# Optimization experiments

Measured on AMD Instinct MI355X. Metric: run time of the kernel, lower is better.

Reference implementation:

```python
import jax, jax.numpy as jnp
import numpy as np

VAR0, VAR1 = 0.1, 0.2
THRESHOLD = 0.35
NEGPOS_RATIO = 7
LOW_GT_THRESH = 0.2  # match() filters GT whose best prior IoU < 0.2


def setup_inputs() -> dict:
    key = jax.random.key(0)
    ks = jax.random.split(key, 8)
    B, P, G = 16, 43008, 128
    loc_data = jax.random.normal(ks[0], (B, P, 4), jnp.float32)
    conf_data = jax.random.normal(ks[1], (B, P, 2), jnp.float32)
    landm_data = jax.random.normal(ks[2], (B, P, 10), jnp.float32)
    # priors in cxcywh form, positive sizes
    pc = jax.random.uniform(ks[3], (P, 2), jnp.float32)
    pwh = jax.random.uniform(ks[4], (P, 2), jnp.float32, minval=0.02, maxval=0.32)
    priors = jnp.concatenate([pc, pwh], axis=1)
    # targets: valid xyxy boxes + 10 landmark coords + label (face=1)
    ctr = jax.random.uniform(ks[5], (B, G, 2), jnp.float32, minval=0.2, maxval=0.8)
    wh = jax.random.uniform(ks[6], (B, G, 2), jnp.float32, minval=0.05, maxval=0.3)
    boxes = jnp.concatenate([ctr - wh / 2, ctr + wh / 2], axis=-1)
    landms = jax.random.uniform(ks[7], (B, G, 10), jnp.float32)
    labels = jnp.ones((B, G, 1), jnp.float32)
    targets = jnp.concatenate([boxes, landms, labels], axis=-1)
    return {"loc_data": loc_data, "conf_data": conf_data, "landm_data": landm_data,
            "priors": priors, "targets": targets}


def point_form(priors):
    return jnp.concatenate([priors[:, :2] - priors[:, 2:] / 2,
                            priors[:, :2] + priors[:, 2:] / 2], axis=1)


def jaccard(a, b):  # a: [G,4] xyxy, b: [P,4] xyxy -> [G,P]
    lt = jnp.maximum(a[:, None, :2], b[None, :, :2])
    rb = jnp.minimum(a[:, None, 2:], b[None, :, 2:])
    wh = jnp.clip(rb - lt, 0.0)
    inter = wh[..., 0] * wh[..., 1]
    area_a = (a[:, 2] - a[:, 0]) * (a[:, 3] - a[:, 1])
    area_b = (b[:, 2] - b[:, 0]) * (b[:, 3] - b[:, 1])
    return inter / (area_a[:, None] + area_b[None, :] - inter)


def encode(matched, priors):  # matched xyxy [P,4], priors cxcywh [P,4]
    g_cxcy = (matched[:, :2] + matched[:, 2:]) / 2 - priors[:, :2]
    g_cxcy = g_cxcy / (VAR0 * priors[:, 2:])
    g_wh = jnp.log((matched[:, 2:] - matched[:, :2]) / priors[:, 2:]) / VAR1
    return jnp.concatenate([g_cxcy, g_wh], axis=1)


def encode_landm(matched, priors):  # matched [P,10], priors [P,4]
    m = matched.reshape(-1, 5, 2)
    g = (m - priors[:, None, :2]) / (VAR0 * priors[:, None, 2:])
    return g.reshape(-1, 10)


def match_one(truths, labels, landms, priors):
    G = truths.shape[0]
    overlaps = jaccard(truths, point_form(priors))  # [G, P]
    best_prior_overlap = overlaps.max(axis=1)       # [G]
    best_prior_idx = overlaps.argmax(axis=1)        # [G]
    valid = best_prior_overlap >= LOW_GT_THRESH
    any_valid = jnp.any(valid)
    best_truth_overlap = overlaps.max(axis=0)       # [P]
    best_truth_idx = overlaps.argmax(axis=0)        # [P]
    # index_fill_(0, best_prior_idx_filter, 2): ensure each valid GT keeps its best prior
    fill_val = jnp.where(valid, 2.0, best_truth_overlap[best_prior_idx])
    best_truth_overlap = best_truth_overlap.at[best_prior_idx].set(fill_val)
    # best_truth_idx[best_prior_idx[j]] = j for all j
    best_truth_idx = best_truth_idx.at[best_prior_idx].set(jnp.arange(G))
    matches = truths[best_truth_idx]                       # [P,4]
    conf = labels[best_truth_idx].astype(jnp.int32)        # [P]
    conf = jnp.where(best_truth_overlap < THRESHOLD, 0, conf)
    conf = jnp.where(any_valid, conf, 0)  # no valid GT -> all background
    loc = encode(matches, priors)
    landm = encode_landm(landms[best_truth_idx], priors)
    return loc, conf, landm


def smooth_l1(x):
    ax = jnp.abs(x)
    return jnp.where(ax < 1.0, 0.5 * ax * ax, ax - 0.5)


def reference(loc_data, conf_data, landm_data, priors, targets):
    truths = targets[..., :4]
    landms = targets[..., 4:14]
    labels = targets[..., 14]
    loc_t, conf_t, landm_t = jax.vmap(
        lambda t, l, lm: match_one(t, l, lm, priors))(truths, labels, landms)

    # landmark loss over positives
    pos1 = conf_t > 0
    N1 = jnp.maximum(pos1.sum().astype(jnp.float32), 1.0)
    loss_landm = jnp.sum(smooth_l1(landm_data - landm_t) * pos1[..., None])

    # localization loss over positives
    pos = conf_t != 0
    num_pos = pos.sum(axis=1, keepdims=True)  # [B,1]
    loss_l = jnp.sum(smooth_l1(loc_data - loc_t) * pos[..., None])

    # hard negative mining on per-prior CE loss
    lse = jax.scipy.special.logsumexp(conf_data, axis=-1)  # [B,P]
    gathered = jnp.take_along_axis(conf_data, conf_t[..., None], axis=-1)[..., 0]
    ce_all = lse - gathered                                # [B,P] per-prior CE
    mine = jnp.where(pos, 0.0, ce_all)
    loss_idx = jnp.argsort(-mine, axis=1)
    idx_rank = jnp.argsort(loss_idx, axis=1)
    num_neg = jnp.clip(NEGPOS_RATIO * num_pos, None, pos.shape[1] - 1)
    neg = idx_rank < num_neg
    sel = pos | neg
    loss_c = jnp.sum(jnp.where(sel, ce_all, 0.0))

    N = jnp.maximum(num_pos.sum().astype(jnp.float32), 1.0)
    return loss_l / N, loss_c / N, loss_landm / N1
```

## Files before the change

### kernel.cpp

```cpp
#include <hip/hip_runtime.h>
#include <stdint.h>


#define GC 8
#define PPI 4

__device__ __forceinline__ float sl1(float x) {
  float a = fabsf(x);
  return a < 1.f ? 0.5f * a * a : a - 0.5f;
}

__device__ __forceinline__ double dwave(double v) {
#pragma unroll
  for (int o = 32; o; o >>= 1) v += __shfl_down(v, o);
  return v;
}

__global__ __launch_bounds__(256) void k_mm(
    const float* __restrict__ priors, const float* __restrict__ targets,
    const float* __restrict__ loc, const float* __restrict__ conf,
    const float* __restrict__ lm, float* __restrict__ bto,
    int* __restrict__ bti, unsigned long long* __restrict__ bp,
    float* __restrict__ mine, double* __restrict__ pll,
    double* __restrict__ pllm, double* __restrict__ plc,
    double* __restrict__ msum, int* __restrict__ pnp, int P, int G, int NIOU,
    int PTI, int NGC, int PC) {
  int tid = threadIdx.x;
  __shared__ char smem[16384];
  __shared__ float4 sgt[128];
  __shared__ float sga[128];

  if ((int)blockIdx.x < NIOU) {
    float* st = (float*)smem;
    double* rs = (double*)(smem + 7680);
    int* ri = (int*)(smem + 7808);
    int b = blockIdx.x / PTI, tile = blockIdx.x % PTI;
    int base = tile * (256 * PPI);
    for (int i = tid; i < G * 15; i += 256)
      st[i] = targets[(size_t)b * G * 15 + i];
    for (int g = tid; g < G; g += 256) {
      const float* t = targets + ((size_t)b * G + g) * 15;
      float x1 = t[0], y1 = t[1], x2 = t[2], y2 = t[3];
      sgt[g] = make_float4(x1, y1, x2, y2);
      sga[g] = (x2 - x1) * (y2 - y1);
    }
    __syncthreads();

    float px1[PPI], py1[PPI], px2[PPI], py2[PPI], pa[PPI];
    float bi[PPI], sb[PPI];
    int bidx[PPI];
#pragma unroll
    for (int k = 0; k < PPI; ++k) {
      int p = base + tid + k * 256;
      int pl = p < P ? p : P - 1;
      float4 pr = ((const float4*)priors)[pl];
      px1[k] = pr.x - pr.z * 0.5f; py1[k] = pr.y - pr.w * 0.5f;
      px2[k] = pr.x + pr.z * 0.5f; py2[k] = pr.y + pr.w * 0.5f;
      pa[k] = pr.z * pr.w;
      bi[k] = 0.f; sb[k] = 1.f; bidx[k] = 0;
    }

#define IOU_BODY(T, A, GG)                                                 \
  {                                                                        \
    float iw = fminf(T.z, px2[k]) - fmaxf(T.x, px1[k]);                    \
    float ih = fminf(T.w, py2[k]) - fmaxf(T.y, py1[k]);                    \
    float inter = fmaxf(iw, 0.f) * ih;                                     \
    float S = A + pa[k];                                                   \
    if (inter * sb[k] > bi[k] * S) { bi[k] = inter; sb[k] = S; bidx[k] = GG; } \
  }
    for (int g = 0; g < G; g += 4) {
      float4 T0 = sgt[g], T1 = sgt[g + 1], T2 = sgt[g + 2], T3 = sgt[g + 3];
      float A0 = sga[g], A1 = sga[g + 1], A2 = sga[g + 2], A3 = sga[g + 3];
#pragma unroll
      for (int k = 0; k < PPI; ++k) {
        IOU_BODY(T0, A0, g)
        IOU_BODY(T1, A1, g + 1)
        IOU_BODY(T2, A2, g + 2)
        IOU_BODY(T3, A3, g + 3)
      }
    }
#undef IOU_BODY

    double ll = 0, llm = 0, lc = 0, ms = 0;
    int np = 0;
#pragma unroll
    for (int k = 0; k < PPI; ++k) {
      int p = base + tid + k * 256;
      if (p < P) {
        size_t idx = (size_t)b * P + p;
        float ov = bi[k] / (sb[k] - bi[k]);
        int ti = bidx[k];
        bto[idx] = ov;
        bti[idx] = ti;
        bool pos = ov >= 0.35f;
        float2 c = ((const float2*)conf)[idx];
        float mx = fmaxf(c.x, c.y);
        float dd = fabsf(c.x - c.y);
        float lse = mx + logf(1.f + expf(-dd));
        float ce = lse - (pos ? c.y : c.x);
        float mv = pos ? 0.f : ce;
        mine[idx] = mv;
        ms += (double)mv;
        if (pos) {
          np++;
          lc += (double)ce;
          float4 pr = ((const float4*)priors)[p];
          const float* t = st + ti * 15;
          float rz = 1.f / pr.z, rw = 1.f / pr.w;
          float rdx = 10.f * rz, rdy = 10.f * rw;
          float gx = ((t[0] + t[2]) * 0.5f - pr.x) * rdx;
          float gy = ((t[1] + t[3]) * 0.5f - pr.y) * rdy;
          float gw = logf((t[2] - t[0]) * rz) * 5.0f;
          float gh = logf((t[3] - t[1]) * rw) * 5.0f;
          float4 ld = ((const float4*)loc)[idx];
          ll += (double)(sl1(ld.x - gx) + sl1(ld.y - gy) + sl1(ld.z - gw) +
                         sl1(ld.w - gh));
          const float2* lmd = (const float2*)lm + idx * 5;
          float s = 0.f;
#pragma unroll
          for (int j = 0; j < 5; ++j) {
            float2 lv = lmd[j];
            float ex = (t[4 + 2 * j] - pr.x) * rdx;
            float ey = (t[5 + 2 * j] - pr.y) * rdy;
            s += sl1(lv.x - ex) + sl1(lv.y - ey);
          }
          llm += (double)s;
        }
      }
    }

    ll = dwave(ll); llm = dwave(llm); lc = dwave(lc); ms = dwave(ms);
#pragma unroll
    for (int o = 32; o; o >>= 1) np += __shfl_down(np, o);
    int lane = tid & 63, wid = tid >> 6;
    if (lane == 0) {
      rs[wid] = ll; rs[4 + wid] = llm; rs[8 + wid] = lc; rs[12 + wid] = ms;
      ri[wid] = np;
    }
    __syncthreads();
    if (tid == 0) {
      pll[blockIdx.x] = rs[0] + rs[1] + rs[2] + rs[3];
      pllm[blockIdx.x] = rs[4] + rs[5] + rs[6] + rs[7];
      plc[blockIdx.x] = rs[8] + rs[9] + rs[10] + rs[11];
      msum[blockIdx.x] = rs[12] + rs[13] + rs[14] + rs[15];
      pnp[blockIdx.x] = ri[0] + ri[1] + ri[2] + ri[3];
    }
  } else {
    unsigned long long* sred = (unsigned long long*)smem;
    int bc = blockIdx.x - NIOU;
    int pc = bc % PC;
    int gcb = (bc / PC) % NGC;
    int b = bc / (PC * NGC);
    int g0 = gcb * GC;

    if (tid < GC) {
      int g = g0 + tid;
      float4 v = make_float4(0.f, 0.f, 0.f, 0.f);
      if (g < G) {
        const float* t = targets + ((size_t)b * G + g) * 15;
        v = make_float4(t[0], t[1], t[2], t[3]);
      }
      sgt[tid] = v;
    }
    __syncthreads();

    float gx1[GC], gy1[GC], gx2[GC], gy2[GC], ga[GC];
#pragma unroll
    for (int j = 0; j < GC; ++j) {
      float4 T = sgt[j];
      gx1[j] = T.x; gy1[j] = T.y; gx2[j] = T.z; gy2[j] = T.w;
      ga[j] = (T.z - T.x) * (T.w - T.y);
    }

    int chunk = (P + PC - 1) / PC;
    int ps = pc * chunk;
    int pe = ps + chunk; if (pe > P) pe = P;
    int count = pe - ps;

    float bi[GC], sb[GC];
    unsigned bpp[GC];
#pragma unroll
    for (int j = 0; j < GC; ++j) { bi[j] = 0.f; sb[j] = 1.f; bpp[j] = (unsigned)(ps + tid); }

#define BP_BODY(X1, Y1, X2, Y2, AR, PP)                                     \
  {                                                                         \
    float iw = fminf(gx2[j], X2) - fmaxf(gx1[j], X1);                       \
    float ih = fminf(gy2[j], Y2) - fmaxf(gy1[j], Y1);                       \
    float inter = fmaxf(iw, 0.f) * ih;                                      \
    float S = ga[j] + AR;                                                   \
    if (inter * sb[j] > bi[j] * S) { bi[j] = inter; sb[j] = S; bpp[j] = (unsigned)PP; } \
  }
    for (int i = tid; i < count; i += 1024) {
      int p0 = ps + i;
      int i1 = i + 256, i2 = i + 512, i3 = i + 768;
      int p1 = (i1 < count) ? ps + i1 : p0;
      int p2 = (i2 < count) ? ps + i2 : p0;
      int p3 = (i3 < count) ? ps + i3 : p0;
      float4 q0 = ((const float4*)priors)[p0];
      float4 q1 = ((const float4*)priors)[p1];
      float4 q2 = ((const float4*)priors)[p2];
      float4 q3 = ((const float4*)priors)[p3];
      float ax1 = q0.x - q0.z * 0.5f, ay1 = q0.y - q0.w * 0.5f;
      float ax2 = q0.x + q0.z * 0.5f, ay2 = q0.y + q0.w * 0.5f;
      float aa = q0.z * q0.w;
      float bx1 = q1.x - q1.z * 0.5f, by1 = q1.y - q1.w * 0.5f;
      float bx2 = q1.x + q1.z * 0.5f, by2 = q1.y + q1.w * 0.5f;
      float ba = q1.z * q1.w;
      float cx1 = q2.x - q2.z * 0.5f, cy1 = q2.y - q2.w * 0.5f;
      float cx2 = q2.x + q2.z * 0.5f, cy2 = q2.y + q2.w * 0.5f;
      float ca = q2.z * q2.w;
      float dx1 = q3.x - q3.z * 0.5f, dy1 = q3.y - q3.w * 0.5f;
      float dx2 = q3.x + q3.z * 0.5f, dy2 = q3.y + q3.w * 0.5f;
      float da = q3.z * q3.w;
#pragma unroll
      for (int j = 0; j < GC; ++j) {
        BP_BODY(ax1, ay1, ax2, ay2, aa, p0)
        BP_BODY(bx1, by1, bx2, by2, ba, p1)
        BP_BODY(cx1, cy1, cx2, cy2, ca, p2)
        BP_BODY(dx1, dy1, dx2, dy2, da, p3)
      }
    }
#undef BP_BODY

#pragma unroll
    for (int j = 0; j < GC; ++j) {
      float iou = bi[j] / (sb[j] - bi[j]);
      unsigned long long pk =
          ((unsigned long long)__float_as_uint(iou) << 32) | (unsigned)(~bpp[j]);
      sred[j * 256 + tid] = pk;
    }
    __syncthreads();
    {
      int j = tid >> 5, s = tid & 31;
      unsigned long long m = sred[j * 256 + s];
#pragma unroll
      for (int t = 1; t < 8; ++t) {
        unsigned long long v = sred[j * 256 + s + t * 32];
        if (v > m) m = v;
      }
      __syncthreads();
      sred[j * 256 + s] = m;
    }
    __syncthreads();
    if (tid < GC) {
      unsigned long long m = sred[tid * 256];
      for (int s = 1; s < 32; ++s) {
        unsigned long long v = sred[tid * 256 + s];
        if (v > m) m = v;
      }
      int g = g0 + tid;
      if (g < G) atomicMax(&bp[(size_t)b * G + g], m);
    }
  }
}

__global__ void k_fix(const unsigned long long* __restrict__ bp,
                      const float* __restrict__ bto, const int* __restrict__ bti,
                      const float* __restrict__ conf, const float* __restrict__ loc,
                      const float* __restrict__ lm, const float* __restrict__ priors,
                      const float* __restrict__ targets, float* __restrict__ mine,
                      int* __restrict__ anyv, double* __restrict__ dacc,
                      int* __restrict__ dnpb, int P, int G) {
  int b = blockIdx.x, g = threadIdx.x;
  __shared__ unsigned spp[128];
  __shared__ double sd[128 * 4];
  __shared__ int si[128];

  unsigned long long m = bp[(size_t)b * G + g];
  unsigned pp = ~(unsigned)m;
  float val = __uint_as_float((unsigned)(m >> 32));
  spp[g] = pp;
  bool valid = val >= 0.2f;
  int av = __syncthreads_or(valid ? 1 : 0);
  if (g == 0) anyv[b] = av;

  bool win = true;
  for (int g2 = g + 1; g2 < G; ++g2)
    if (spp[g2] == pp) { win = false; break; }

  double dll = 0, dllm = 0, dlc = 0, dms = 0;
  int dnp = 0;
  if (win) {
    size_t idx = (size_t)b * P + pp;
    float ov_o = bto[idx];
    int ti_o = bti[idx];
    float ov_n = valid ? 2.0f : ov_o;
    int ti_n = g;
    bool pos_o = ov_o >= 0.35f, pos_n = ov_n >= 0.35f;

    float2 c = ((const float2*)conf)[idx];
    float mx = fmaxf(c.x, c.y);
    float dd = fabsf(c.x - c.y);
    float lse = mx + logf(1.f + expf(-dd));
    float ce_o = lse - (pos_o ? c.y : c.x);
    float ce_n = lse - (pos_n ? c.y : c.x);
    float mv_o = mine[idx];
    float mv_n = pos_n ? 0.f : ce_n;
    if (mv_n != mv_o) mine[idx] = mv_n;
    dms = (double)mv_n - (double)mv_o;
    dnp = (pos_n ? 1 : 0) - (pos_o ? 1 : 0);
    dlc = (pos_n ? (double)ce_n : 0.0) - (pos_o ? (double)ce_o : 0.0);

    if (pos_o || pos_n) {
      float4 pr = ((const float4*)priors)[pp];
      float rz = 1.f / pr.z, rw = 1.f / pr.w;
      float rdx = 10.f * rz, rdy = 10.f * rw;
      float4 ld = ((const float4*)loc)[idx];
      const float2* lmd = (const float2*)lm + idx * 5;
      float2 lv[5];
#pragma unroll
      for (int j = 0; j < 5; ++j) lv[j] = lmd[j];
      for (int pass = 0; pass < 2; ++pass) {
        bool act = pass ? pos_n : pos_o;
        int ti = pass ? ti_n : ti_o;
        if (!act) continue;
        const float* t = targets + ((size_t)b * G + ti) * 15;
        float gx = ((t[0] + t[2]) * 0.5f - pr.x) * rdx;
        float gy = ((t[1] + t[3]) * 0.5f - pr.y) * rdy;
        float gw = logf((t[2] - t[0]) * rz) * 5.0f;
        float gh = logf((t[3] - t[1]) * rw) * 5.0f;
        double l = (double)(sl1(ld.x - gx) + sl1(ld.y - gy) +
                            sl1(ld.z - gw) + sl1(ld.w - gh));
        float s = 0.f;
#pragma unroll
        for (int j = 0; j < 5; ++j) {
          float ex = (t[4 + 2 * j] - pr.x) * rdx;
          float ey = (t[5 + 2 * j] - pr.y) * rdy;
          s += sl1(lv[j].x - ex) + sl1(lv[j].y - ey);
        }
        if (pass) { dll += l; dllm += (double)s; }
        else { dll -= l; dllm -= (double)s; }
      }
    }
  }
  sd[g] = dll; sd[128 + g] = dllm; sd[256 + g] = dlc; sd[384 + g] = dms;
  si[g] = dnp;
  __syncthreads();
  for (int off = 64; off; off >>= 1) {
    if (g < off) {
      sd[g] += sd[g + off]; sd[128 + g] += sd[128 + g + off];
      sd[256 + g] += sd[256 + g + off]; sd[384 + g] += sd[384 + g + off];
      si[g] += si[g + off];
    }
    __syncthreads();
  }
  if (g == 0) {
    dacc[b * 4 + 0] = sd[0]; dacc[b * 4 + 1] = sd[128];
    dacc[b * 4 + 2] = sd[256]; dacc[b * 4 + 3] = sd[384];
    dnpb[b] = si[0];
  }
}

__global__ __launch_bounds__(1024) void k_tail(
    const int* __restrict__ pnp, const double* __restrict__ msum,
    const double* __restrict__ pll, const double* __restrict__ pllm,
    const double* __restrict__ plc, const double* __restrict__ dacc,
    const int* __restrict__ dnpb, const int* __restrict__ anyv,
    const float* __restrict__ mine, int* __restrict__ num_pos,
    double* __restrict__ pllb, double* __restrict__ pllmb,
    double* __restrict__ plcb, double* __restrict__ pfs_b, int P, int PTI) {
  int b = blockIdx.x, tid = threadIdx.x;
  __shared__ double rs[16 * 5];
  __shared__ int ris[16];
  __shared__ unsigned S[1024];
  __shared__ unsigned hs[2048];
  __shared__ int spf1, sk1, spf21, sk2;
  __shared__ unsigned stb;
  __shared__ double stie;

  double a = 0, cc = 0, d = 0, ms = 0;
  int n = 0;
  for (int i = tid; i < PTI; i += 1024) {
    int ix = b * PTI + i;
    a += pll[ix]; cc += pllm[ix]; d += plc[ix]; ms += msum[ix]; n += pnp[ix];
  }
  a = dwave(a); cc = dwave(cc); d = dwave(d); ms = dwave(ms);
#pragma unroll
  for (int o = 32; o; o >>= 1) n += __shfl_down(n, o);
  int lane = tid & 63, wid = tid >> 6;
  if (lane == 0) {
    rs[wid] = a; rs[16 + wid] = cc; rs[32 + wid] = d; rs[48 + wid] = ms;
    ris[wid] = n;
  }
  __syncthreads();
  int npos = 0;
  double A = 0, C = 0, D = 0, MS = 0;
  if (tid == 0) {
    for (int i = 0; i < 16; ++i) {
      A += rs[i]; C += rs[16 + i]; D += rs[32 + i]; MS += rs[48 + i];
      npos += ris[i];
    }
    A += dacc[b * 4 + 0]; C += dacc[b * 4 + 1]; D += dacc[b * 4 + 2];
    MS += dacc[b * 4 + 3];
    npos += dnpb[b];
    if (!anyv[b]) { A = 0; C = 0; D = 0; npos = 0; }
    num_pos[b] = npos;
    pllb[b] = A; pllmb[b] = C; plcb[b] = D;
    ris[0] = npos;
    rs[48] = MS;
  }
  __syncthreads();
  npos = ris[0];
  MS = rs[48];

  long long k = 7LL * (long long)npos;
  long long cap = P - 1;
  if (k <= 0) {
    if (tid == 0) pfs_b[b] = 0.0;
    return;
  }
  if (k >= cap) {
    if (tid == 0) pfs_b[b] = MS;
    return;
  }

  const float* mrow = mine + (size_t)b * P;
  hs[tid] = 0;
  __syncthreads();
  for (int base = 0; base < P; base += 4096) {
    int i0 = base + tid;
    int i1 = i0 + 1024, i2 = i0 + 2048, i3 = i0 + 3072;
    unsigned b0 = (i0 < P) ? __float_as_uint(mrow[i0]) : 0xFFFFFFFFu;
    unsigned b1 = (i1 < P) ? __float_as_uint(mrow[i1]) : 0xFFFFFFFFu;
    unsigned b2 = (i2 < P) ? __float_as_uint(mrow[i2]) : 0xFFFFFFFFu;
    unsigned b3 = (i3 < P) ? __float_as_uint(mrow[i3]) : 0xFFFFFFFFu;
    if (b0 != 0xFFFFFFFFu) atomicAdd(&hs[b0 >> 21], 1u);
    if (b1 != 0xFFFFFFFFu) atomicAdd(&hs[b1 >> 21], 1u);
    if (b2 != 0xFFFFFFFFu) atomicAdd(&hs[b2 >> 21], 1u);
    if (b3 != 0xFFFFFFFFu) atomicAdd(&hs[b3 >> 21], 1u);
  }
  __syncthreads();
  {
    S[tid] = hs[tid];
    __syncthreads();
    for (int off = 1; off < 1024; off <<= 1) {
      unsigned add = (tid + off < 1024) ? S[tid + off] : 0;
      __syncthreads();
      S[tid] += add;
      __syncthreads();
    }
    int cnt = __syncthreads_count((long long)S[tid] >= k);
    int seg = cnt - 1;
    if (tid == seg) {
      long long cum = (seg + 1 < 1024) ? (long long)S[seg + 1] : 0;
      spf1 = seg;
      sk1 = (int)(k - cum);
    }
  }
  __syncthreads();
  int pf = spf1;

  hs[tid] = 0; hs[tid + 1024] = 0;
  __syncthreads();
  for (int base = 0; base < P; base += 4096) {
    int i0 = base + tid;
    int i1 = i0 + 1024, i2 = i0 + 2048, i3 = i0 + 3072;
    unsigned b0 = (i0 < P) ? __float_as_uint(mrow[i0]) : 0u;
    unsigned b1 = (i1 < P) ? __float_as_uint(mrow[i1]) : 0u;
    unsigned b2 = (i2 < P) ? __float_as_uint(mrow[i2]) : 0u;
    unsigned b3 = (i3 < P) ? __float_as_uint(mrow[i3]) : 0u;
    if (i0 < P && (int)(b0 >> 21) == pf) atomicAdd(&hs[(b0 >> 10) & 2047], 1u);
    if (i1 < P && (int)(b1 >> 21) == pf) atomicAdd(&hs[(b1 >> 10) & 2047], 1u);
    if (i2 < P && (int)(b2 >> 21) == pf) atomicAdd(&hs[(b2 >> 10) & 2047], 1u);
    if (i3 < P && (int)(b3 >> 21) == pf) atomicAdd(&hs[(b3 >> 10) & 2047], 1u);
  }
  __syncthreads();
  {
    unsigned h0 = hs[tid * 2], h1v = hs[tid * 2 + 1];
    S[tid] = h0 + h1v;
    __syncthreads();
    for (int off = 1; off < 1024; off <<= 1) {
      unsigned add = (tid + off < 1024) ? S[tid + off] : 0;
      __syncthreads();
      S[tid] += add;
      __syncthreads();
    }
    long long kk = (long long)sk1;
    int cnt = __syncthreads_count((long long)S[tid] >= kk);
    int seg = cnt - 1;
    if (tid == seg) {
      long long cum = (seg + 1 < 1024) ? (long long)S[seg + 1] : 0;
      int bin = seg * 2;
      if (cum + h1v >= kk) bin = seg * 2 + 1;
      else cum += h1v;
      spf21 = (pf << 11) | bin;
      sk2 = (int)(kk - cum);
    }
  }
  __syncthreads();
  int pf21 = spf21;

  hs[tid] = 0;
  __syncthreads();
  for (int base = 0; base < P; base += 4096) {
    int i0 = base + tid;
    int i1 = i0 + 1024, i2 = i0 + 2048, i3 = i0 + 3072;
    unsigned b0 = (i0 < P) ? __float_as_uint(mrow[i0]) : 0u;
    unsigned b1 = (i1 < P) ? __float_as_uint(mrow[i1]) : 0u;
    unsigned b2 = (i2 < P) ? __float_as_uint(mrow[i2]) : 0u;
    unsigned b3 = (i3 < P) ? __float_as_uint(mrow[i3]) : 0u;
    if (i0 < P && (int)(b0 >> 10) == pf21) atomicAdd(&hs[b0 & 1023], 1u);
    if (i1 < P && (int)(b1 >> 10) == pf21) atomicAdd(&hs[b1 & 1023], 1u);
    if (i2 < P && (int)(b2 >> 10) == pf21) atomicAdd(&hs[b2 & 1023], 1u);
    if (i3 < P && (int)(b3 >> 10) == pf21) atomicAdd(&hs[b3 & 1023], 1u);
  }
  __syncthreads();
  {
    S[tid] = hs[tid];
    __syncthreads();
    for (int off = 1; off < 1024; off <<= 1) {
      unsigned add = (tid + off < 1024) ? S[tid + off] : 0;
      __syncthreads();
      S[tid] += add;
      __syncthreads();
    }
    long long kk = (long long)sk2;
    int cnt = __syncthreads_count((long long)S[tid] >= kk);
    int seg = cnt - 1;
    if (tid == seg) {
      long long cum = (seg + 1 < 1024) ? (long long)S[seg + 1] : 0;
      unsigned tb = ((unsigned)pf21 << 10) | (unsigned)seg;
      stb = tb;
      stie = (double)(kk - cum) * (double)__uint_as_float(tb);
    }
  }
  __syncthreads();

  unsigned tb = stb;
  double v = 0.0;
  for (int base = 0; base < P; base += 4096) {
    int i0 = base + tid;
    int i1 = i0 + 1024, i2 = i0 + 2048, i3 = i0 + 3072;
    unsigned b0 = (i0 < P) ? __float_as_uint(mrow[i0]) : 0u;
    unsigned b1 = (i1 < P) ? __float_as_uint(mrow[i1]) : 0u;
    unsigned b2 = (i2 < P) ? __float_as_uint(mrow[i2]) : 0u;
    unsigned b3 = (i3 < P) ? __float_as_uint(mrow[i3]) : 0u;
    if (b0 > tb) v += (double)__uint_as_float(b0);
    if (b1 > tb) v += (double)__uint_as_float(b1);
    if (b2 > tb) v += (double)__uint_as_float(b2);
    if (b3 > tb) v += (double)__uint_as_float(b3);
  }
  v = dwave(v);
  if (lane == 0) rs[wid] = v;
  __syncthreads();
  if (tid == 0) {
    double t = 0;
    for (int i = 0; i < 16; ++i) t += rs[i];
    pfs_b[b] = t + stie;
  }
}

__global__ void k_fin(const double* __restrict__ pllb,
                      const double* __restrict__ pllmb,
                      const double* __restrict__ plcb,
                      const double* __restrict__ pfs_b,
                      const int* __restrict__ num_pos, float* __restrict__ out,
                      int B) {
  if (threadIdx.x == 0) {
    double A = 0, C = 0, D = 0, F = 0, N = 0;
    for (int i = 0; i < B; ++i) {
      A += pllb[i]; C += pllmb[i]; D += plcb[i]; F += pfs_b[i];
      N += (double)num_pos[i];
    }
    if (N < 1.0) N = 1.0;
    out[0] = (float)(A / N);
    out[1] = (float)((D + F) / N);
    out[2] = (float)(C / N);
  }
}

extern "C" void kernel_launch(void* const* d_in, const int* in_sizes, int n_in,
                              void* d_out, int out_size, void* d_ws,
                              size_t ws_size, hipStream_t stream) {
  const float* loc = (const float*)d_in[0];
  const float* conf = (const float*)d_in[1];
  const float* lm = (const float*)d_in[2];
  const float* priors = (const float*)d_in[3];
  const float* targets = (const float*)d_in[4];

  int P = in_sizes[3] / 4;
  int B = in_sizes[0] / (4 * P);
  int G = in_sizes[4] / (15 * B);
  int PTI = (P + 256 * PPI - 1) / (256 * PPI);
  int NIOU = B * PTI;
  int NGC = (G + GC - 1) / GC;
  int PC = 8;
  int NBP = B * NGC * PC;

  char* w = (char*)d_ws;
  size_t off = 0;
  unsigned long long* bp = (unsigned long long*)(w + off);
  off += (size_t)B * G * 8;
  size_t clear_bytes = off;
  off = (off + 255) & ~(size_t)255;
  float* bto = (float*)(w + off);
  off += (size_t)B * P * 4;
  int* bti = (int*)(w + off);
  off += (size_t)B * P * 4;
  float* mine = (float*)(w + off);
  off += (size_t)B * P * 4;
  double* pll = (double*)(w + off);
  off += (size_t)NIOU * 8;
  double* pllm = (double*)(w + off);
  off += (size_t)NIOU * 8;
  double* plc = (double*)(w + off);
  off += (size_t)NIOU * 8;
  double* msum = (double*)(w + off);
  off += (size_t)NIOU * 8;
  int* pnp = (int*)(w + off);
  off += (size_t)NIOU * 4;
  off = (off + 7) & ~(size_t)7;
  double* dacc = (double*)(w + off);
  off += (size_t)B * 4 * 8;
  double* pllb = (double*)(w + off);
  off += (size_t)B * 8;
  double* pllmb = (double*)(w + off);
  off += (size_t)B * 8;
  double* plcb = (double*)(w + off);
  off += (size_t)B * 8;
  double* pfs_b = (double*)(w + off);
  off += (size_t)B * 8;
  int* dnpb = (int*)(w + off);
  off += (size_t)B * 4;
  int* anyv = (int*)(w + off);
  off += (size_t)B * 4;
  int* num_pos = (int*)(w + off);
  off += (size_t)B * 4;

  hipMemsetAsync(d_ws, 0, clear_bytes, stream);

  k_mm<<<NIOU + NBP, 256, 0, stream>>>(priors, targets, loc, conf, lm, bto,
                                       bti, bp, mine, pll, pllm, plc, msum,
                                       pnp, P, G, NIOU, PTI, NGC, PC);
  k_fix<<<B, G, 0, stream>>>(bp, bto, bti, conf, loc, lm, priors, targets,
                             mine, anyv, dacc, dnpb, P, G);
  k_tail<<<B, 1024, 0, stream>>>(pnp, msum, pll, pllm, plc, dacc, dnpb, anyv,
                                 mine, num_pos, pllb, pllmb, plcb, pfs_b, P,
                                 PTI);
  k_fin<<<1, 64, 0, stream>>>(pllb, pllmb, plcb, pfs_b, num_pos,
                              (float*)d_out, B);
}
```

Before: 177.1 us.

## Build top-level histogram in main kernel and compact candidates for radix select

```diff
diff --git a/kernel.cpp b/kernel.cpp
--- a/kernel.cpp
+++ b/kernel.cpp
@@ -21,10 +21,10 @@
     const float* __restrict__ loc, const float* __restrict__ conf,
     const float* __restrict__ lm, float* __restrict__ bto,
     int* __restrict__ bti, unsigned long long* __restrict__ bp,
-    float* __restrict__ mine, double* __restrict__ pll,
-    double* __restrict__ pllm, double* __restrict__ plc,
-    double* __restrict__ msum, int* __restrict__ pnp, int P, int G, int NIOU,
-    int PTI, int NGC, int PC) {
+    float* __restrict__ mine, unsigned* __restrict__ ghist,
+    double* __restrict__ pll, double* __restrict__ pllm,
+    double* __restrict__ plc, double* __restrict__ msum,
+    int* __restrict__ pnp, int P, int G, int NIOU, int PTI, int NGC, int PC) {
   int tid = threadIdx.x;
   __shared__ char smem[16384];
   __shared__ float4 sgt[128];
@@ -34,6 +34,7 @@
     float* st = (float*)smem;
     double* rs = (double*)(smem + 7680);
     int* ri = (int*)(smem + 7808);
+    unsigned* hist = (unsigned*)(smem + 8192);
     int b = blockIdx.x / PTI, tile = blockIdx.x % PTI;
     int base = tile * (256 * PPI);
     for (int i = tid; i < G * 15; i += 256)
@@ -44,6 +45,7 @@
       sgt[g] = make_float4(x1, y1, x2, y2);
       sga[g] = (x2 - x1) * (y2 - y1);
     }
+    for (int i = tid; i < 1024; i += 256) hist[i] = 0;
     __syncthreads();
 
     float px1[PPI], py1[PPI], px2[PPI], py2[PPI], pa[PPI];
@@ -100,6 +102,7 @@
         float ce = lse - (pos ? c.y : c.x);
         float mv = pos ? 0.f : ce;
         mine[idx] = mv;
+        atomicAdd(&hist[__float_as_uint(mv) >> 21], 1u);
         ms += (double)mv;
         if (pos) {
           np++;
@@ -144,6 +147,10 @@
       plc[blockIdx.x] = rs[8] + rs[9] + rs[10] + rs[11];
       msum[blockIdx.x] = rs[12] + rs[13] + rs[14] + rs[15];
       pnp[blockIdx.x] = ri[0] + ri[1] + ri[2] + ri[3];
+    }
+    for (int i = tid; i < 1024; i += 256) {
+      unsigned c = hist[i];
+      if (c) atomicAdd(&ghist[b * 1024 + i], c);
     }
   } else {
     unsigned long long* sred = (unsigned long long*)smem;
@@ -254,38 +261,51 @@
   }
 }
 
-__global__ void k_fix(const unsigned long long* __restrict__ bp,
-                      const float* __restrict__ bto, const int* __restrict__ bti,
-                      const float* __restrict__ conf, const float* __restrict__ loc,
-                      const float* __restrict__ lm, const float* __restrict__ priors,
-                      const float* __restrict__ targets, float* __restrict__ mine,
-                      int* __restrict__ anyv, double* __restrict__ dacc,
-                      int* __restrict__ dnpb, int P, int G) {
-  int b = blockIdx.x, g = threadIdx.x;
+__global__ __launch_bounds__(1024) void k_selfix(
+    const unsigned long long* __restrict__ bp, const float* __restrict__ bto,
+    const int* __restrict__ bti, const float* __restrict__ conf,
+    const float* __restrict__ loc, const float* __restrict__ lm,
+    const float* __restrict__ priors, const float* __restrict__ targets,
+    float* __restrict__ mine, unsigned* __restrict__ ghist,
+    const int* __restrict__ pnp, const double* __restrict__ msum,
+    const double* __restrict__ pll, const double* __restrict__ pllm,
+    const double* __restrict__ plc, int* __restrict__ num_pos,
+    double* __restrict__ pllb, double* __restrict__ pllmb,
+    double* __restrict__ plcb, int* __restrict__ selstate,
+    double* __restrict__ pfs_b, int P, int G, int PTI) {
+  int b = blockIdx.x, tid = threadIdx.x;
   __shared__ unsigned spp[128];
-  __shared__ double sd[128 * 4];
-  __shared__ int si[128];
-
-  unsigned long long m = bp[(size_t)b * G + g];
-  unsigned pp = ~(unsigned)m;
-  float val = __uint_as_float((unsigned)(m >> 32));
-  spp[g] = pp;
-  bool valid = val >= 0.2f;
-  int av = __syncthreads_or(valid ? 1 : 0);
-  if (g == 0) anyv[b] = av;
-
-  bool win = true;
-  for (int g2 = g + 1; g2 < G; ++g2)
-    if (spp[g2] == pp) { win = false; break; }
+  __shared__ double rs[16 * 5];
+  __shared__ int ris[16];
+  __shared__ unsigned S[1024];
+  __shared__ double sdel[4];
+  __shared__ int sdnp, sav, smode;
+  __shared__ long long sk;
 
   double dll = 0, dllm = 0, dlc = 0, dms = 0;
   int dnp = 0;
+  unsigned pp = 0;
+  bool valid = false;
+  if (tid < G) {
+    unsigned long long m = bp[(size_t)b * G + tid];
+    pp = ~(unsigned)m;
+    float val = __uint_as_float((unsigned)(m >> 32));
+    spp[tid] = pp;
+    valid = val >= 0.2f;
+  }
+  int av = __syncthreads_or((tid < G && valid) ? 1 : 0);
+  bool win = false;
+  if (tid < G) {
+    win = true;
+    for (int g2 = tid + 1; g2 < G; ++g2)
+      if (spp[g2] == pp) { win = false; break; }
+  }
   if (win) {
     size_t idx = (size_t)b * P + pp;
     float ov_o = bto[idx];
     int ti_o = bti[idx];
     float ov_n = valid ? 2.0f : ov_o;
-    int ti_n = g;
+    int ti_n = tid;
     bool pos_o = ov_o >= 0.35f, pos_n = ov_n >= 0.35f;
 
     float2 c = ((const float2*)conf)[idx];
@@ -296,7 +316,11 @@
     float ce_n = lse - (pos_n ? c.y : c.x);
     float mv_o = mine[idx];
     float mv_n = pos_n ? 0.f : ce_n;
-    if (mv_n != mv_o) mine[idx] = mv_n;
+    if (mv_n != mv_o) {
+      mine[idx] = mv_n;
+      atomicSub(&ghist[b * 1024 + (__float_as_uint(mv_o) >> 21)], 1u);
+      atomicAdd(&ghist[b * 1024 + (__float_as_uint(mv_n) >> 21)], 1u);
+    }
     dms = (double)mv_n - (double)mv_o;
     dnp = (pos_n ? 1 : 0) - (pos_o ? 1 : 0);
     dlc = (pos_n ? (double)ce_n : 0.0) - (pos_o ? (double)ce_o : 0.0);
@@ -333,40 +357,26 @@
       }
     }
   }
-  sd[g] = dll; sd[128 + g] = dllm; sd[256 + g] = dlc; sd[384 + g] = dms;
-  si[g] = dnp;
-  __syncthreads();
-  for (int off = 64; off; off >>= 1) {
-    if (g < off) {
-      sd[g] += sd[g + off]; sd[128 + g] += sd[128 + g + off];
-      sd[256 + g] += sd[256 + g + off]; sd[384 + g] += sd[384 + g + off];
-      si[g] += si[g + off];
-    }
-    __syncthreads();
-  }
-  if (g == 0) {
-    dacc[b * 4 + 0] = sd[0]; dacc[b * 4 + 1] = sd[128];
-    dacc[b * 4 + 2] = sd[256]; dacc[b * 4 + 3] = sd[384];
-    dnpb[b] = si[0];
-  }
-}
-
-__global__ __launch_bounds__(1024) void k_tail(
-    const int* __restrict__ pnp, const double* __restrict__ msum,
-    const double* __restrict__ pll, const double* __restrict__ pllm,
-    const double* __restrict__ plc, const double* __restrict__ dacc,
-    const int* __restrict__ dnpb, const int* __restrict__ anyv,
-    const float* __restrict__ mine, int* __restrict__ num_pos,
-    double* __restrict__ pllb, double* __restrict__ pllmb,
-    double* __restrict__ plcb, double* __restrict__ pfs_b, int P, int PTI) {
-  int b = blockIdx.x, tid = threadIdx.x;
-  __shared__ double rs[16 * 5];
-  __shared__ int ris[16];
-  __shared__ unsigned S[1024];
-  __shared__ unsigned hs[2048];
-  __shared__ int spf1, sk1, spf21, sk2;
-  __shared__ unsigned stb;
-  __shared__ double stie;
+  dll = dwave(dll); dllm = dwave(dllm); dlc = dwave(dlc); dms = dwave(dms);
+#pragma unroll
+  for (int o = 32; o; o >>= 1) dnp += __shfl_down(dnp, o);
+  int lane = tid & 63, wid = tid >> 6;
+  if (lane == 0) {
+    rs[wid] = dll; rs[16 + wid] = dllm; rs[32 + wid] = dlc; rs[48 + wid] = dms;
+    ris[wid] = dnp;
+  }
+  __syncthreads();
+  if (tid == 0) {
+    double a = 0, c2 = 0, d2 = 0, m2 = 0;
+    int n2 = 0;
+    for (int i = 0; i < 16; ++i) {
+      a += rs[i]; c2 += rs[16 + i]; d2 += rs[32 + i]; m2 += rs[48 + i];
+      n2 += ris[i];
+    }
+    sdel[0] = a; sdel[1] = c2; sdel[2] = d2; sdel[3] = m2;
+    sdnp = n2; sav = av;
+  }
+  __syncthreads();
 
   double a = 0, cc = 0, d = 0, ms = 0;
   int n = 0;
@@ -377,61 +387,116 @@
   a = dwave(a); cc = dwave(cc); d = dwave(d); ms = dwave(ms);
 #pragma unroll
   for (int o = 32; o; o >>= 1) n += __shfl_down(n, o);
-  int lane = tid & 63, wid = tid >> 6;
   if (lane == 0) {
     rs[wid] = a; rs[16 + wid] = cc; rs[32 + wid] = d; rs[48 + wid] = ms;
     ris[wid] = n;
   }
   __syncthreads();
-  int npos = 0;
-  double A = 0, C = 0, D = 0, MS = 0;
   if (tid == 0) {
+    double A = 0, C = 0, D = 0, MS = 0;
+    int npos = 0;
     for (int i = 0; i < 16; ++i) {
       A += rs[i]; C += rs[16 + i]; D += rs[32 + i]; MS += rs[48 + i];
       npos += ris[i];
     }
-    A += dacc[b * 4 + 0]; C += dacc[b * 4 + 1]; D += dacc[b * 4 + 2];
-    MS += dacc[b * 4 + 3];
-    npos += dnpb[b];
-    if (!anyv[b]) { A = 0; C = 0; D = 0; npos = 0; }
+    A += sdel[0]; C += sdel[1]; D += sdel[2]; MS += sdel[3];
+    npos += sdnp;
+    if (!sav) { A = 0; C = 0; D = 0; npos = 0; }
     num_pos[b] = npos;
     pllb[b] = A; pllmb[b] = C; plcb[b] = D;
-    ris[0] = npos;
-    rs[48] = MS;
-  }
-  __syncthreads();
-  npos = ris[0];
-  MS = rs[48];
-
-  long long k = 7LL * (long long)npos;
-  long long cap = P - 1;
-  if (k <= 0) {
-    if (tid == 0) pfs_b[b] = 0.0;
-    return;
-  }
-  if (k >= cap) {
-    if (tid == 0) pfs_b[b] = MS;
-    return;
-  }
-
-  const float* mrow = mine + (size_t)b * P;
-  hs[tid] = 0;
-  __syncthreads();
-  for (int base = 0; base < P; base += 4096) {
-    int i0 = base + tid;
-    int i1 = i0 + 1024, i2 = i0 + 2048, i3 = i0 + 3072;
-    unsigned b0 = (i0 < P) ? __float_as_uint(mrow[i0]) : 0xFFFFFFFFu;
-    unsigned b1 = (i1 < P) ? __float_as_uint(mrow[i1]) : 0xFFFFFFFFu;
-    unsigned b2 = (i2 < P) ? __float_as_uint(mrow[i2]) : 0xFFFFFFFFu;
-    unsigned b3 = (i3 < P) ? __float_as_uint(mrow[i3]) : 0xFFFFFFFFu;
-    if (b0 != 0xFFFFFFFFu) atomicAdd(&hs[b0 >> 21], 1u);
-    if (b1 != 0xFFFFFFFFu) atomicAdd(&hs[b1 >> 21], 1u);
-    if (b2 != 0xFFFFFFFFu) atomicAdd(&hs[b2 >> 21], 1u);
-    if (b3 != 0xFFFFFFFFu) atomicAdd(&hs[b3 >> 21], 1u);
+    long long k = 7LL * (long long)npos;
+    long long cap = P - 1;
+    int md = 1;
+    if (k <= 0) { pfs_b[b] = 0.0; selstate[2 * b] = -1; md = 0; }
+    else if (k >= cap) { pfs_b[b] = MS; selstate[2 * b] = -1; md = 0; }
+    smode = md; sk = k;
+  }
+  __syncthreads();
+  if (!smode) return;
+  long long k = sk;
+
+  S[tid] = ghist[b * 1024 + tid];
+  __syncthreads();
+  for (int off = 1; off < 1024; off <<= 1) {
+    unsigned add = (tid + off < 1024) ? S[tid + off] : 0;
+    __syncthreads();
+    S[tid] += add;
+    __syncthreads();
+  }
+  int cnt_ = __syncthreads_count((long long)S[tid] >= k);
+  int seg = cnt_ - 1;
+  if (tid == seg) {
+    long long cum = (seg + 1 < 1024) ? (long long)S[seg + 1] : 0;
+    selstate[2 * b] = seg;
+    selstate[2 * b + 1] = (int)(k - cum);
+  }
+}
+
+__global__ __launch_bounds__(256) void k_compact(
+    const int* __restrict__ selstate, const float* __restrict__ mine,
+    float* __restrict__ cbuf, unsigned* __restrict__ cntb,
+    double* __restrict__ part_hi, int P, int NCC) {
+  int b = blockIdx.x / NCC, blk = blockIdx.x % NCC;
+  int t = selstate[2 * b];
+  if (t < 0) return;
+  __shared__ unsigned lcnt, lbase;
+  __shared__ double sa[4];
+  if (threadIdx.x == 0) lcnt = 0;
+  __syncthreads();
+  int base = blk * 1024;
+  double acc = 0;
+  float keep[4];
+  int nk = 0;
+  for (int i = threadIdx.x; i < 1024; i += 256) {
+    int p = base + i;
+    if (p < P) {
+      unsigned bb = __float_as_uint(mine[(size_t)b * P + p]);
+      int bin = (int)(bb >> 21);
+      if (bin > t) acc += (double)__uint_as_float(bb);
+      else if (bin == t) keep[nk++] = __uint_as_float(bb);
+    }
+  }
+  unsigned myoff = nk ? atomicAdd(&lcnt, (unsigned)nk) : 0u;
+  __syncthreads();
+  if (threadIdx.x == 0) lbase = lcnt ? atomicAdd(&cntb[b], lcnt) : 0u;
+  __syncthreads();
+  unsigned wb = lbase + myoff;
+  for (int j = 0; j < nk; ++j) cbuf[(size_t)b * P + wb + j] = keep[j];
+  acc = dwave(acc);
+  int lane = threadIdx.x & 63, wid = threadIdx.x >> 6;
+  if (lane == 0) sa[wid] = acc;
+  __syncthreads();
+  if (threadIdx.x == 0)
+    part_hi[(size_t)b * NCC + blk] = sa[0] + sa[1] + sa[2] + sa[3];
+}
+
+__global__ __launch_bounds__(1024) void k_sel2(
+    const int* __restrict__ selstate, const float* __restrict__ cbuf,
+    const unsigned* __restrict__ cntb, const double* __restrict__ part_hi,
+    double* __restrict__ pfs_b, int P, int NCC) {
+  int b = blockIdx.x, tid = threadIdx.x;
+  int t = selstate[2 * b];
+  if (t < 0) return;
+  long long k1 = (long long)selstate[2 * b + 1];
+  int n = (int)cntb[b];
+  const float* row = cbuf + (size_t)b * P;
+  __shared__ unsigned hs[2048];
+  __shared__ unsigned S[1024];
+  __shared__ double rs[16];
+  __shared__ int spf21, sk2;
+  __shared__ unsigned stb;
+  __shared__ double stie;
+
+  hs[tid] = 0; hs[tid + 1024] = 0;
+  __syncthreads();
+  for (int i = tid; i < n; i += 1024) {
+    unsigned bb = __float_as_uint(row[i]);
+    atomicAdd(&hs[(bb >> 10) & 2047], 1u);
   }
   __syncthreads();
   {
-    S[tid] = hs[tid];
+    unsigned h0 = hs[tid * 2], h1v = hs[tid * 2 + 1];
+    S[tid] = h0 + h1v;
     __syncthreads();
     for (int off = 1; off < 1024; off <<= 1) {
       unsigned add = (tid + off < 1024) ? S[tid + off] : 0;
@@ -439,35 +504,29 @@
       S[tid] += add;
       __syncthreads();
     }
-    int cnt = __syncthreads_count((long long)S[tid] >= k);
-    int seg = cnt - 1;
+    int cnt_ = __syncthreads_count((long long)S[tid] >= k1);
+    int seg = cnt_ - 1;
     if (tid == seg) {
       long long cum = (seg + 1 < 1024) ? (long long)S[seg + 1] : 0;
-      spf1 = seg;
-      sk1 = (int)(k - cum);
-    }
-  }
-  __syncthreads();
-  int pf = spf1;
-
-  hs[tid] = 0; hs[tid + 1024] = 0;
-  __syncthreads();
-  for (int base = 0; base < P; base += 4096) {
-    int i0 = base + tid;
-    int i1 = i0 + 1024, i2 = i0 + 2048, i3 = i0 + 3072;
-    unsigned b0 = (i0 < P) ? __float_as_uint(mrow[i0]) : 0u;
-    unsigned b1 = (i1 < P) ? __float_as_uint(mrow[i1]) : 0u;
-    unsigned b2 = (i2 < P) ? __float_as_uint(mrow[i2]) : 0u;
-    unsigned b3 = (i3 < P) ? __float_as_uint(mrow[i3]) : 0u;
-    if (i0 < P && (int)(b0 >> 21) == pf) atomicAdd(&hs[(b0 >> 10) & 2047], 1u);
-    if (i1 < P && (int)(b1 >> 21) == pf) atomicAdd(&hs[(b1 >> 10) & 2047], 1u);
-    if (i2 < P && (int)(b2 >> 21) == pf) atomicAdd(&hs[(b2 >> 10) & 2047], 1u);
-    if (i3 < P && (int)(b3 >> 21) == pf) atomicAdd(&hs[(b3 >> 10) & 2047], 1u);
+      int bin = seg * 2;
+      if (cum + h1v >= k1) bin = seg * 2 + 1;
+      else cum += h1v;
+      spf21 = (t << 11) | bin;
+      sk2 = (int)(k1 - cum);
+    }
+  }
+  __syncthreads();
+  int pf21 = spf21;
+
+  hs[tid] = 0;
+  __syncthreads();
+  for (int i = tid; i < n; i += 1024) {
+    unsigned bb = __float_as_uint(row[i]);
+    if ((int)(bb >> 10) == pf21) atomicAdd(&hs[bb & 1023], 1u);
   }
   __syncthreads();
   {
-    unsigned h0 = hs[tid * 2], h1v = hs[tid * 2 + 1];
-    S[tid] = h0 + h1v;
+    S[tid] = hs[tid];
     __syncthreads();
     for (int off = 1; off < 1024; off <<= 1) {
       unsigned add = (tid + off < 1024) ? S[tid + off] : 0;
@@ -475,48 +534,9 @@
       S[tid] += add;
       __syncthreads();
     }
-    long long kk = (long long)sk1;
-    int cnt = __syncthreads_count((long long)S[tid] >= kk);
-    int seg = cnt - 1;
-    if (tid == seg) {
-      long long cum = (seg + 1 < 1024) ? (long long)S[seg + 1] : 0;
-      int bin = seg * 2;
-      if (cum + h1v >= kk) bin = seg * 2 + 1;
-      else cum += h1v;
-      spf21 = (pf << 11) | bin;
-      sk2 = (int)(kk - cum);
-    }
-  }
-  __syncthreads();
-  int pf21 = spf21;
-
-  hs[tid] = 0;
-  __syncthreads();
-  for (int base = 0; base < P; base += 4096) {
-    int i0 = base + tid;
-    int i1 = i0 + 1024, i2 = i0 + 2048, i3 = i0 + 3072;
-    unsigned b0 = (i0 < P) ? __float_as_uint(mrow[i0]) : 0u;
-    unsigned b1 = (i1 < P) ? __float_as_uint(mrow[i1]) : 0u;
-    unsigned b2 = (i2 < P) ? __float_as_uint(mrow[i2]) : 0u;
-    unsigned b3 = (i3 < P) ? __float_as_uint(mrow[i3]) : 0u;
-    if (i0 < P && (int)(b0 >> 10) == pf21) atomicAdd(&hs[b0 & 1023], 1u);
-    if (i1 < P && (int)(b1 >> 10) == pf21) atomicAdd(&hs[b1 & 1023], 1u);
-    if (i2 < P && (int)(b2 >> 10) == pf21) atomicAdd(&hs[b2 & 1023], 1u);
-    if (i3 < P && (int)(b3 >> 10) == pf21) atomicAdd(&hs[b3 & 1023], 1u);
-  }
-  __syncthreads();
-  {
-    S[tid] = hs[tid];
-    __syncthreads();
-    for (int off = 1; off < 1024; off <<= 1) {
-      unsigned add = (tid + off < 1024) ? S[tid + off] : 0;
-      __syncthreads();
-      S[tid] += add;
-      __syncthreads();
-    }
     long long kk = (long long)sk2;
-    int cnt = __syncthreads_count((long long)S[tid] >= kk);
-    int seg = cnt - 1;
+    int cnt_ = __syncthreads_count((long long)S[tid] >= kk);
+    int seg = cnt_ - 1;
     if (tid == seg) {
       long long cum = (seg + 1 < 1024) ? (long long)S[seg + 1] : 0;
       unsigned tb = ((unsigned)pf21 << 10) | (unsigned)seg;
@@ -528,25 +548,20 @@
 
   unsigned tb = stb;
   double v = 0.0;
-  for (int base = 0; base < P; base += 4096) {
-    int i0 = base + tid;
-    int i1 = i0 + 1024, i2 = i0 + 2048, i3 = i0 + 3072;
-    unsigned b0 = (i0 < P) ? __float_as_uint(mrow[i0]) : 0u;
-    unsigned b1 = (i1 < P) ? __float_as_uint(mrow[i1]) : 0u;
-    unsigned b2 = (i2 < P) ? __float_as_uint(mrow[i2]) : 0u;
-    unsigned b3 = (i3 < P) ? __float_as_uint(mrow[i3]) : 0u;
-    if (b0 > tb) v += (double)__uint_as_float(b0);
-    if (b1 > tb) v += (double)__uint_as_float(b1);
-    if (b2 > tb) v += (double)__uint_as_float(b2);
-    if (b3 > tb) v += (double)__uint_as_float(b3);
+  for (int i = tid; i < n; i += 1024) {
+    unsigned bb = __float_as_uint(row[i]);
+    if (bb > tb) v += (double)__uint_as_float(bb);
   }
   v = dwave(v);
+  int lane = tid & 63, wid = tid >> 6;
   if (lane == 0) rs[wid] = v;
   __syncthreads();
   if (tid == 0) {
-    double t = 0;
-    for (int i = 0; i < 16; ++i) t += rs[i];
-    pfs_b[b] = t + stie;
+    double hi = 0;
+    for (int j = 0; j < NCC; ++j) hi += part_hi[(size_t)b * NCC + j];
+    double tot = 0;
+    for (int i = 0; i < 16; ++i) tot += rs[i];
+    pfs_b[b] = hi + tot + stie;
   }
 }
 
@@ -586,11 +601,16 @@
   int NGC = (G + GC - 1) / GC;
   int PC = 8;
   int NBP = B * NGC * PC;
+  int NCC = (P + 1023) / 1024;
 
   char* w = (char*)d_ws;
   size_t off = 0;
   unsigned long long* bp = (unsigned long long*)(w + off);
   off += (size_t)B * G * 8;
+  unsigned* ghist = (unsigned*)(w + off);
+  off += (size_t)B * 1024 * 4;
+  unsigned* cntb = (unsigned*)(w + off);
+  off += (size_t)B * 4;
   size_t clear_bytes = off;
   off = (off + 255) & ~(size_t)255;
   float* bto = (float*)(w + off);
@@ -610,8 +630,8 @@
   int* pnp = (int*)(w + off);
   off += (size_t)NIOU * 4;
   off = (off + 7) & ~(size_t)7;
-  double* dacc = (double*)(w + off);
-  off += (size_t)B * 4 * 8;
+  double* part_hi = (double*)(w + off);
+  off += (size_t)B * NCC * 8;
   double* pllb = (double*)(w + off);
   off += (size_t)B * 8;
   double* pllmb = (double*)(w + off);
@@ -620,23 +640,23 @@
   off += (size_t)B * 8;
   double* pfs_b = (double*)(w + off);
   off += (size_t)B * 8;
-  int* dnpb = (int*)(w + off);
-  off += (size_t)B * 4;
-  int* anyv = (int*)(w + off);
-  off += (size_t)B * 4;
+  int* selstate = (int*)(w + off);
+  off += (size_t)B * 2 * 4;
   int* num_pos = (int*)(w + off);
   off += (size_t)B * 4;
 
   hipMemsetAsync(d_ws, 0, clear_bytes, stream);
 
   k_mm<<<NIOU + NBP, 256, 0, stream>>>(priors, targets, loc, conf, lm, bto,
-                                       bti, bp, mine, pll, pllm, plc, msum,
-                                       pnp, P, G, NIOU, PTI, NGC, PC);
-  k_fix<<<B, G, 0, stream>>>(bp, bto, bti, conf, loc, lm, priors, targets,
-                             mine, anyv, dacc, dnpb, P, G);
-  k_tail<<<B, 1024, 0, stream>>>(pnp, msum, pll, pllm, plc, dacc, dnpb, anyv,
-                                 mine, num_pos, pllb, pllmb, plcb, pfs_b, P,
-                                 PTI);
+                                       bti, bp, mine, ghist, pll, pllm, plc,
+                                       msum, pnp, P, G, NIOU, PTI, NGC, PC);
+  k_selfix<<<B, 1024, 0, stream>>>(bp, bto, bti, conf, loc, lm, priors,
+                                   targets, mine, ghist, pnp, msum, pll, pllm,
+                                   plc, num_pos, pllb, pllmb, plcb, selstate,
+                                   pfs_b, P, G, PTI);
+  k_compact<<<B * NCC, 256, 0, stream>>>(selstate, mine, bto, cntb, part_hi,
+                                         P, NCC);
+  k_sel2<<<B, 1024, 0, stream>>>(selstate, bto, cntb, part_hi, pfs_b, P, NCC);
   k_fin<<<1, 64, 0, stream>>>(pllb, pllmb, plcb, pfs_b, num_pos,
                               (float*)d_out, B);
 }
```

Result: slower. 181.2 us (+2.3%).
